# Kernel optimization log

Measured on AMD Instinct MI355X. Metric: run time of the kernel, lower is better.

Reference implementation:

```python
import jax, jax.numpy as jnp
import numpy as np
from jax import lax

DIM = 2048
N_HEADS = 16
N_KV = 4
HEAD_DIM = DIM // N_HEADS  # 128
ROPE_BASE = 10000.0
SEQ = 4096
BSZ = 1


def bitlinear(x, W):
    # per-row abs-mean scale (detached), ternary round/clamp, straight-through blend
    s = lax.stop_gradient(jnp.clip(jnp.mean(jnp.abs(W), axis=1, keepdims=True), 1e-5, None))
    wt = jnp.clip(jnp.round(W / s), -1.0, 1.0)
    w = lax.stop_gradient(wt - W) + W  # straight-through
    return x @ (w * s).T


def rms_norm(x):
    eps = jnp.finfo(x.dtype).eps
    return x * lax.rsqrt(jnp.mean(x * x, axis=-1, keepdims=True) + eps)


def rope(x, cos, sin):
    half = x.shape[-1] // 2
    x1, x2 = x[..., :half], x[..., half:]
    return jnp.concatenate((x1 * cos + x2 * sin, -x1 * sin + x2 * cos), axis=-1)


def setup_inputs() -> dict:
    key = jax.random.key(0)
    ks = jax.random.split(key, 6)
    kv_dim = N_KV * HEAD_DIM
    return {
        "x": jax.random.normal(ks[0], (BSZ, SEQ, DIM), dtype=jnp.float32),
        "wq": jax.random.normal(ks[1], (DIM, DIM), dtype=jnp.float32) * 0.02,
        "wk": jax.random.normal(ks[2], (kv_dim, DIM), dtype=jnp.float32) * 0.02,
        "wv": jax.random.normal(ks[3], (kv_dim, DIM), dtype=jnp.float32) * 0.02,
        "wp": jax.random.normal(ks[4], (DIM, DIM), dtype=jnp.float32) * 0.02,
        "q_gain": jnp.ones((N_HEADS,), dtype=jnp.float32),
    }


def reference(x, wq, wk, wv, wp, q_gain):
    b, s, d = x.shape
    q = bitlinear(x, wq).reshape(b, s, N_HEADS, HEAD_DIM).transpose(0, 2, 1, 3)  # bhsd
    k = bitlinear(x, wk).reshape(b, s, N_KV, HEAD_DIM).transpose(0, 2, 1, 3)
    v = bitlinear(x, wv).reshape(b, s, N_KV, HEAD_DIM).transpose(0, 2, 1, 3)

    q = rms_norm(q)
    k = rms_norm(k)

    inv_freq = 1.0 / ROPE_BASE ** (jnp.arange(0, HEAD_DIM, 2, dtype=jnp.float32) / HEAD_DIM)
    t = jnp.arange(s, dtype=jnp.float32)
    freqs = jnp.outer(t, inv_freq)  # [s, hd/2]
    cos = jnp.cos(freqs)[None, None].astype(q.dtype)
    sin = jnp.sin(freqs)[None, None].astype(q.dtype)
    q = rope(q, cos, sin)
    k = rope(k, cos, sin)

    q = q * q_gain.astype(q.dtype)[None, :, None, None]

    groups = N_HEADS // N_KV
    k = jnp.repeat(k, groups, axis=1)  # GQA expand to [b, H, s, hd]
    v = jnp.repeat(v, groups, axis=1)

    scale = 1.0 / np.sqrt(HEAD_DIM)
    scores = jnp.einsum("bhqd,bhkd->bhqk", q, k) * scale
    causal = jnp.tril(jnp.ones((s, s), dtype=bool))
    scores = jnp.where(causal[None, None], scores, jnp.finfo(scores.dtype).min)
    attn = jax.nn.softmax(scores, axis=-1)
    y = jnp.einsum("bhqk,bhkd->bhqd", attn, v)

    y = y.transpose(0, 2, 1, 3).reshape(b, s, d)
    return bitlinear(y, wp)
```

## Files before the change

### kernel.cpp

```cpp
#include <hip/hip_runtime.h>
#include <math.h>

typedef unsigned short u16;
typedef short s16x8 __attribute__((ext_vector_type(8)));
typedef short s16x4 __attribute__((ext_vector_type(4)));
typedef float f32x4 __attribute__((ext_vector_type(4)));
typedef u16 u16x4 __attribute__((ext_vector_type(4)));

static constexpr size_t OFF_XB   = 0;
static constexpr size_t OFF_WQKV = 16777216;
static constexpr size_t OFF_KH   = 16777216;
static constexpr size_t OFF_VT   = 20971520;
static constexpr size_t OFF_ML   = 25165824;
static constexpr size_t OFF_WP   = 29360128;
static constexpr size_t OFF_QKV  = 37748736;
static constexpr size_t OFF_Y    = 79691776;

__device__ __forceinline__ u16 f2bf(float f) {
  union { float f; unsigned u; } v; v.f = f;
  unsigned r = v.u + 0x7fffu + ((v.u >> 16) & 1u);
  return (u16)(r >> 16);
}

__device__ __forceinline__ float bf2f(u16 b) {
  union { unsigned u; float f; } v; v.u = ((unsigned)b) << 16;
  return v.f;
}

__device__ __forceinline__ void async16(const u16* g, u16* lds) {
  __builtin_amdgcn_global_load_lds(
      (const __attribute__((address_space(1))) void*)g,
      (__attribute__((address_space(3))) void*)lds, 16, 0, 0);
}

__global__ __launch_bounds__(256) void quant_all(const float* __restrict__ wq,
                                                 const float* __restrict__ wk,
                                                 const float* __restrict__ wv,
                                                 const float* __restrict__ wp,
                                                 u16* __restrict__ outqkv,
                                                 u16* __restrict__ outp) {
  const int row = blockIdx.x, tid = threadIdx.x;
  const float* src;
  u16* dst;
  if (row < 2048)      { src = wq + (size_t)row * 2048;          dst = outqkv + (size_t)row * 2048; }
  else if (row < 2560) { src = wk + (size_t)(row - 2048) * 2048; dst = outqkv + (size_t)row * 2048; }
  else if (row < 3072) { src = wv + (size_t)(row - 2560) * 2048; dst = outqkv + (size_t)row * 2048; }
  else                 { src = wp + (size_t)(row - 3072) * 2048; dst = outp + (size_t)(row - 3072) * 2048; }
  src += tid * 8;
  float4 a = *(const float4*)(src);
  float4 b = *(const float4*)(src + 4);
  float asum = fabsf(a.x)+fabsf(a.y)+fabsf(a.z)+fabsf(a.w)
             + fabsf(b.x)+fabsf(b.y)+fabsf(b.z)+fabsf(b.w);
  #pragma unroll
  for (int off = 1; off < 64; off <<= 1) asum += __shfl_xor(asum, off, 64);
  __shared__ float red[4];
  if ((tid & 63) == 0) red[tid >> 6] = asum;
  __syncthreads();
  float s = fmaxf((red[0]+red[1]+red[2]+red[3]) * (1.0f/2048.0f), 1e-5f);
  float v[8] = {a.x,a.y,a.z,a.w,b.x,b.y,b.z,b.w};
  u16* d = dst + tid * 8;
  #pragma unroll
  for (int i = 0; i < 8; i++) {
    float q = rintf(v[i] / s);
    q = fminf(fmaxf(q, -1.f), 1.f);
    d[i] = f2bf(q * s);
  }
}

__global__ __launch_bounds__(256) void cvt_bf16(const float* __restrict__ in,
                                                u16* __restrict__ out) {
  size_t i = ((size_t)blockIdx.x * 256 + threadIdx.x) * 4;
  float4 v = *(const float4*)(in + i);
  u16x4 o;
  o.x = f2bf(v.x); o.y = f2bf(v.y); o.z = f2bf(v.z); o.w = f2bf(v.w);
  *(u16x4*)(out + i) = o;
}

__global__ __launch_bounds__(256) void gemm_bt(const u16* __restrict__ A,
                                               const u16* __restrict__ B,
                                               float* __restrict__ C,
                                               int M, int N, int K) {
  __shared__ u16 sA[128 * 32];
  __shared__ u16 sB[128 * 32];
  const int tid = threadIdx.x;
  const int lane = tid & 63;
  const int wid = tid >> 6;
  const int lr = lane & 15, lq = lane >> 4;
  const int wm = (wid >> 1) * 64, wn = (wid & 1) * 64;
  const size_t m0 = (size_t)blockIdx.y * 128, n0 = (size_t)blockIdx.x * 128;

  const int r0 = tid >> 2, c0 = (tid & 3) * 8;
  const u16* Ab0 = A + (m0 + r0) * (size_t)K + c0;
  const u16* Ab1 = A + (m0 + 64 + r0) * (size_t)K + c0;
  const u16* Bb0 = B + (n0 + r0) * (size_t)K + c0;
  const u16* Bb1 = B + (n0 + 64 + r0) * (size_t)K + c0;
  u16* sA0 = &sA[tid * 8];
  u16* sA1 = &sA[(256 + tid) * 8];
  u16* sB0 = &sB[tid * 8];
  u16* sB1 = &sB[(256 + tid) * 8];

  f32x4 acc[4][4] = {};

  for (int kt = 0; kt < K; kt += 32) {
    async16(Ab0 + kt, sA0);
    async16(Ab1 + kt, sA1);
    async16(Bb0 + kt, sB0);
    async16(Bb1 + kt, sB1);
    __syncthreads();
    s16x8 af[4], bf[4];
    #pragma unroll
    for (int mt = 0; mt < 4; mt++)
      af[mt] = *(const s16x8*)&sA[(wm + mt * 16 + lr) * 32 + lq * 8];
    #pragma unroll
    for (int nt = 0; nt < 4; nt++)
      bf[nt] = *(const s16x8*)&sB[(wn + nt * 16 + lr) * 32 + lq * 8];
    #pragma unroll
    for (int mt = 0; mt < 4; mt++)
      #pragma unroll
      for (int nt = 0; nt < 4; nt++)
        acc[mt][nt] = __builtin_amdgcn_mfma_f32_16x16x32_bf16(af[mt], bf[nt], acc[mt][nt], 0, 0, 0);
    __syncthreads();
  }
  #pragma unroll
  for (int mt = 0; mt < 4; mt++)
    #pragma unroll
    for (int nt = 0; nt < 4; nt++)
      #pragma unroll
      for (int r = 0; r < 4; r++) {
        size_t m = m0 + wm + mt * 16 + lq * 4 + r;
        size_t n = n0 + wn + nt * 16 + lr;
        C[m * (size_t)N + n] = acc[mt][nt][r];
      }
}

__global__ __launch_bounds__(256) void prep_qk(const float* __restrict__ qkv,
                                               const float* __restrict__ qgain,
                                               u16* __restrict__ Qh,
                                               u16* __restrict__ Kh) {
  const int s = blockIdx.y;
  const int j = blockIdx.x * 4 + (threadIdx.x >> 6);
  const int t = threadIdx.x & 63;
  const float* row = qkv + (size_t)s * 3072 + (size_t)j * 128;
  float x1 = row[t], x2 = row[t + 64];
  float ss = x1 * x1 + x2 * x2;
  #pragma unroll
  for (int off = 1; off < 64; off <<= 1) ss += __shfl_xor(ss, off, 64);
  float rn = rsqrtf(ss * (1.0f / 128.0f) + 1.1920929e-07f);
  float invf = exp2f(-(float)t * 0.20762050593048096f);
  float ang = (float)s * invf;
  float sn, c;
  sincosf(ang, &sn, &c);
  if (j < 16) {
    float g = qgain[j] * 0.12751738f;
    float q1 = x1 * rn, q2 = x2 * rn;
    float o1 = (q1 * c + q2 * sn) * g;
    float o2 = (-q1 * sn + q2 * c) * g;
    u16* dst = Qh + ((size_t)j * 4096 + s) * 128;
    dst[t] = f2bf(o1); dst[t + 64] = f2bf(o2);
  } else {
    const int kvh = j - 16;
    float k1 = x1 * rn, k2 = x2 * rn;
    float o1 = k1 * c + k2 * sn;
    float o2 = -k1 * sn + k2 * c;
    const int tt = s >> 6, kr = s & 63;
    u16* base = Kh + (((size_t)kvh * 64 + tt) * 4) * 2048 + kr * 32 + (t & 31);
    base[(size_t)(t >> 5) * 2048]       = f2bf(o1);
    base[(size_t)(2 + (t >> 5)) * 2048] = f2bf(o2);
  }
}

__global__ __launch_bounds__(256) void vtrans(const float* __restrict__ qkv,
                                              u16* __restrict__ Vtg) {
  __shared__ float tile[64][67];
  const int tid = threadIdx.x;
  const int s0 = blockIdx.y * 64;
  const int c0 = blockIdx.x * 64;
  #pragma unroll
  for (int it = 0; it < 4; it++) {
    int i = it * 256 + tid;
    int r = i >> 4, c = (i & 15) * 4;
    float4 v = *(const float4*)(qkv + (size_t)(s0 + r) * 3072 + 2560 + c0 + c);
    tile[r][c] = v.x; tile[r][c + 1] = v.y; tile[r][c + 2] = v.z; tile[r][c + 3] = v.w;
  }
  __syncthreads();
  #pragma unroll
  for (int it = 0; it < 2; it++) {
    int i = it * 256 + tid;
    int dl = i >> 3, sc = (i & 7) * 8;
    int cglob = c0 + dl;
    int kvh = cglob >> 7, d = cglob & 127;
    int tt = s0 >> 6;
    int a0 = 16 * ((sc >> 2) & 3) + 4 * (sc >> 4);
    int a1 = 16 * (((sc >> 2) + 1) & 3) + 4 * (sc >> 4);
    int x = d & 7;
    int p0 = ((((a0 >> 3) ^ x) << 3) | (a0 & 7));
    int p1 = ((((a1 >> 3) ^ x) << 3) | (a1 & 7));
    size_t rowbase = (((size_t)kvh * 64 + tt) * 128 + d) * 64;
    u16 lo[4], hi[4];
    #pragma unroll
    for (int jj = 0; jj < 4; jj++) lo[jj] = f2bf(tile[sc + jj][dl]);
    #pragma unroll
    for (int jj = 0; jj < 4; jj++) hi[jj] = f2bf(tile[sc + 4 + jj][dl]);
    *(s16x4*)&Vtg[rowbase + p0] = *(s16x4*)lo;
    *(s16x4*)&Vtg[rowbase + p1] = *(s16x4*)hi;
  }
}

#define SEG(qt,a,b,s) ((unsigned)((qt)|((a)<<5)|((b)<<11)|((s)<<18)))
__constant__ unsigned SEGTAB[128] = {
  SEG(0,0,2,127),   SEG(15,0,15,14),
  SEG(15,15,32,15), 0,
  SEG(1,0,4,127),   SEG(14,0,13,12),
  SEG(14,13,30,13), 0,
  SEG(2,0,6,127),   SEG(13,0,11,10),
  SEG(13,11,28,11), 0,
  SEG(3,0,8,127),   SEG(12,0,9,8),
  SEG(12,9,26,9),   0,
  SEG(4,0,10,127),  SEG(11,0,7,6),
  SEG(11,7,24,7),   0,
  SEG(5,0,12,127),  SEG(10,0,5,4),
  SEG(10,5,22,5),   0,
  SEG(6,0,14,127),  SEG(9,0,3,2),
  SEG(9,3,20,3),    0,
  SEG(7,0,16,127),  SEG(8,0,1,0),
  SEG(8,1,18,1),    0,
  SEG(16,0,16,16),  0,
  SEG(16,16,33,17), 0,
  SEG(16,33,34,18), SEG(17,0,15,19),
  SEG(17,15,31,20), 0,
  SEG(17,31,36,21), SEG(18,0,12,22),
  SEG(18,12,28,23), 0,
  SEG(18,28,38,24), SEG(19,0,6,25),
  SEG(19,6,23,26),  0,
  SEG(19,23,39,27), 0,
  SEG(19,39,40,28), SEG(20,0,15,29),
  SEG(20,15,32,30), 0,
  SEG(20,32,42,31), SEG(21,0,6,32),
  SEG(21,6,22,33),  0,
  SEG(21,22,39,34), 0,
  SEG(21,39,44,35), SEG(22,0,11,36),
  SEG(22,11,27,37), 0,
  SEG(22,27,44,38), 0,
  SEG(22,44,46,39), SEG(23,0,14,40),
  SEG(23,14,30,41), 0,
  SEG(23,30,47,42), 0,
  SEG(23,47,48,43), SEG(24,0,15,44),
  SEG(24,15,31,45), 0,
  SEG(24,31,48,46), 0,
  SEG(24,48,50,47), SEG(25,0,14,48),
  SEG(25,14,30,49), 0,
  SEG(25,30,47,50), 0,
  SEG(25,47,52,51), SEG(26,0,11,52),
  SEG(26,11,27,53), 0,
  SEG(26,27,44,54), 0,
  SEG(26,44,54,55), SEG(27,0,6,56),
  SEG(27,6,22,57),  0,
  SEG(27,22,39,58), 0,
  SEG(27,39,55,59), 0,
  SEG(27,55,56,60), SEG(28,0,15,61),
  SEG(28,15,32,62), 0,
  SEG(28,32,48,63), 0,
  SEG(28,48,58,64), SEG(29,0,6,65),
  SEG(29,6,23,66),  0,
  SEG(29,23,39,67), 0,
  SEG(29,39,55,68), 0,
  SEG(29,55,60,69), SEG(30,0,12,70),
  SEG(30,12,28,71), 0,
  SEG(30,28,44,72), 0,
  SEG(30,44,61,73), 0,
  SEG(30,61,62,74), SEG(31,0,15,75),
  SEG(31,15,31,76), 0,
  SEG(31,31,48,77), 0,
  SEG(31,48,64,78), 0,
};
__constant__ unsigned char CBASE[24] = {0,2,4,6,8,10,12,14, 16,19,22,25,29,32,36,40, 44,48,52,56,61,65,70,75};
__constant__ unsigned char CCNT[24]  = {2,2,2,2,2,2,2,2, 3,3,3,4,3,4,4,4, 4,4,4,5,4,5,5,4};

__global__ __launch_bounds__(256, 2) void attn(const u16* __restrict__ Q,
                                               const u16* __restrict__ Kh,
                                               const u16* __restrict__ Vt,
                                               u16* __restrict__ Y,
                                               u16* __restrict__ Opart,
                                               float* __restrict__ MLpart) {
  const int tid = threadIdx.x, lane = tid & 63, wid = tid >> 6;
  const int lr = lane & 15, lq = lane >> 4;
  const int b = blockIdx.x;
  const int h = b & 15, unit = b >> 4;
  const int kvh = h >> 2;

  __shared__ u16 sK[4 * 64 * 32];
  __shared__ u16 sVt[128 * 64];

  const u16* Kbase = Kh + (size_t)kvh * 64 * 8192;
  const u16* Vbase = Vt + (size_t)kvh * 64 * 8192;

  const int o01 = (((2 * lq) ^ (lr & 7)) << 3);
  const int o23 = (((2 * lq + 1) ^ (lr & 7)) << 3);

  #pragma unroll 1
  for (int si = 0; si < 2; ++si) {
    const unsigned sd = SEGTAB[unit * 2 + si];
    const int qt = sd & 31;
    const int t0 = (sd >> 5) & 63;
    const int t1 = (sd >> 11) & 127;
    const int slot = (sd >> 18) & 127;
    if (t1 <= t0) continue;
    const int qbase = qt * 128;

    s16x8 qf[2][4];
    #pragma unroll
    for (int f = 0; f < 2; f++) {
      const u16* qp = Q + ((size_t)h * 4096 + qbase + wid * 32 + f * 16 + lr) * 128 + lq * 8;
      #pragma unroll
      for (int kc = 0; kc < 4; kc++) qf[f][kc] = *(const s16x8*)(qp + kc * 32);
    }

    f32x4 oacc[2][8] = {};
    f32x4 lacc[2] = {};
    float mrow[2] = {-1e30f, -1e30f};

    for (int t = t0; t < t1; ++t) {
      const u16* Kt = Kbase + (size_t)t * 8192;
      const u16* Vtt = Vbase + (size_t)t * 8192;
      #pragma unroll
      for (int it = 0; it < 4; it++) {
        int off = it * 2048 + tid * 8;
        async16(Kt + off, &sK[off]);
        async16(Vtt + off, &sVt[off]);
      }
      __syncthreads();

      f32x4 sacc[2][4] = {};
      #pragma unroll
      for (int nt = 0; nt < 4; nt++)
        #pragma unroll
        for (int kc = 0; kc < 4; kc++) {
          s16x8 kf = *(const s16x8*)&sK[kc * 2048 + (nt * 16 + lr) * 32 + lq * 8];
          sacc[0][nt] = __builtin_amdgcn_mfma_f32_16x16x32_bf16(kf, qf[0][kc], sacc[0][nt], 0, 0, 0);
          sacc[1][nt] = __builtin_amdgcn_mfma_f32_16x16x32_bf16(kf, qf[1][kc], sacc[1][nt], 0, 0, 0);
        }

      if (t >= 2 * qt) {
        #pragma unroll
        for (int f = 0; f < 2; f++) {
          int qg = qbase + wid * 32 + f * 16 + lr;
          #pragma unroll
          for (int nt = 0; nt < 4; nt++) {
            int kv0 = t * 64 + nt * 16 + lq * 4;
            #pragma unroll
            for (int r = 0; r < 4; r++)
              if (kv0 + r > qg) sacc[f][nt][r] = -1e30f;
          }
        }
      }

      float pm[2];
      #pragma unroll
      for (int f = 0; f < 2; f++) {
        float a = fmaxf(fmaxf(sacc[f][0][0], sacc[f][0][1]), fmaxf(sacc[f][0][2], sacc[f][0][3]));
        float bb = fmaxf(fmaxf(sacc[f][1][0], sacc[f][1][1]), fmaxf(sacc[f][1][2], sacc[f][1][3]));
        float cc = fmaxf(fmaxf(sacc[f][2][0], sacc[f][2][1]), fmaxf(sacc[f][2][2], sacc[f][2][3]));
        float dd = fmaxf(fmaxf(sacc[f][3][0], sacc[f][3][1]), fmaxf(sacc[f][3][2], sacc[f][3][3]));
        pm[f] = fmaxf(fmaxf(a, bb), fmaxf(cc, dd));
      }
      if (__any((pm[0] > mrow[0] + 3.0f) || (pm[1] > mrow[1] + 3.0f))) {
        #pragma unroll
        for (int f = 0; f < 2; f++) {
          float mn = pm[f];
          mn = fmaxf(mn, __shfl_xor(mn, 16, 64));
          mn = fmaxf(mn, __shfl_xor(mn, 32, 64));
          mn = fmaxf(mn, mrow[f]);
          float al = exp2f(mrow[f] - mn);
          mrow[f] = mn;
          lacc[f] *= al;
          #pragma unroll
          for (int dt = 0; dt < 8; dt++)
            #pragma unroll
            for (int r = 0; r < 4; r++) oacc[f][dt][r] *= al;
        }
      }

      s16x4 pf[2][4];
      #pragma unroll
      for (int f = 0; f < 2; f++)
        #pragma unroll
        for (int nt = 0; nt < 4; nt++)
          #pragma unroll
          for (int r = 0; r < 4; r++) {
            union { float fv; unsigned u; } pu;
            pu.fv = exp2f(sacc[f][nt][r] - mrow[f]);
            lacc[f][r] += pu.fv;
            pf[f][nt][r] = (short)(pu.u >> 16);
          }

      #pragma unroll
      for (int dt = 0; dt < 8; dt++) {
        const u16* vrow = &sVt[(dt * 16 + lr) * 64];
        s16x8 v01 = *(const s16x8*)(vrow + o01);
        s16x8 v23 = *(const s16x8*)(vrow + o23);
        s16x4 vf0 = {v01[0], v01[1], v01[2], v01[3]};
        s16x4 vf1 = {v01[4], v01[5], v01[6], v01[7]};
        s16x4 vf2 = {v23[0], v23[1], v23[2], v23[3]};
        s16x4 vf3 = {v23[4], v23[5], v23[6], v23[7]};
        #pragma unroll
        for (int f = 0; f < 2; f++) {
          oacc[f][dt] = __builtin_amdgcn_mfma_f32_16x16x16bf16_1k(vf0, pf[f][0], oacc[f][dt], 0, 0, 0);
          oacc[f][dt] = __builtin_amdgcn_mfma_f32_16x16x16bf16_1k(vf1, pf[f][1], oacc[f][dt], 0, 0, 0);
          oacc[f][dt] = __builtin_amdgcn_mfma_f32_16x16x16bf16_1k(vf2, pf[f][2], oacc[f][dt], 0, 0, 0);
          oacc[f][dt] = __builtin_amdgcn_mfma_f32_16x16x16bf16_1k(vf3, pf[f][3], oacc[f][dt], 0, 0, 0);
        }
      }
      __syncthreads();
    }

    float lrow[2];
    #pragma unroll
    for (int f = 0; f < 2; f++) {
      float s4 = (lacc[f][0] + lacc[f][1]) + (lacc[f][2] + lacc[f][3]);
      s4 += __shfl_xor(s4, 16, 64);
      s4 += __shfl_xor(s4, 32, 64);
      lrow[f] = s4;
    }

    if (slot == 127) {
      #pragma unroll
      for (int f = 0; f < 2; f++) {
        float linv = 1.0f / lrow[f];
        int qg = qbase + wid * 32 + f * 16 + lr;
        #pragma unroll
        for (int dt = 0; dt < 8; dt++) {
          u16 tmp[4];
          #pragma unroll
          for (int r = 0; r < 4; r++) tmp[r] = f2bf(oacc[f][dt][r] * linv);
          *(s16x4*)&Y[(size_t)qg * 2048 + h * 128 + dt * 16 + lq * 4] = *(s16x4*)tmp;
        }
      }
    } else {
      const int gslot = h * 79 + slot;
      u16* Op = Opart + (size_t)gslot * 16384;
      #pragma unroll
      for (int f = 0; f < 2; f++) {
        int row = wid * 32 + f * 16 + lr;
        #pragma unroll
        for (int dt = 0; dt < 8; dt++) {
          u16 tmp[4];
          #pragma unroll
          for (int r = 0; r < 4; r++) tmp[r] = f2bf(oacc[f][dt][r]);
          *(s16x4*)&Op[row * 128 + dt * 16 + lq * 4] = *(s16x4*)tmp;
        }
        if (lq == 0) {
          MLpart[(size_t)gslot * 256 + row * 2]     = mrow[f];
          MLpart[(size_t)gslot * 256 + row * 2 + 1] = lrow[f];
        }
      }
    }
  }
}

__global__ __launch_bounds__(256) void combine(const u16* __restrict__ Op,
                                               const float* __restrict__ ML,
                                               u16* __restrict__ Y) {
  const int b = blockIdx.x;
  const int qt = 8 + (b >> 4), h = b & 15;
  const int base = CBASE[qt - 8], n = CCNT[qt - 8];
  const int gbase = h * 79 + base;
  const int tid = threadIdx.x;
  const int row = tid >> 1, half = (tid & 1) * 64;

  float m[5], l[5];
  float mstar = -3e38f;
  for (int i = 0; i < n; i++) {
    m[i] = ML[(size_t)(gbase + i) * 256 + row * 2];
    l[i] = ML[(size_t)(gbase + i) * 256 + row * 2 + 1];
    mstar = fmaxf(mstar, m[i]);
  }
  float w[5], wsum = 0.f;
  for (int i = 0; i < n; i++) { w[i] = exp2f(m[i] - mstar); wsum += l[i] * w[i]; }
  float inv = 1.0f / wsum;

  float acc[64] = {};
  for (int i = 0; i < n; i++) {
    const u16* o = Op + (size_t)(gbase + i) * 16384 + row * 128 + half;
    float wi = w[i];
    #pragma unroll
    for (int c = 0; c < 64; c += 8) {
      s16x8 a = *(const s16x8*)(o + c);
      #pragma unroll
      for (int jj = 0; jj < 8; jj++) acc[c + jj] += wi * bf2f((u16)a[jj]);
    }
  }
  u16* dst = Y + ((size_t)qt * 128 + row) * 2048 + h * 128 + half;
  #pragma unroll
  for (int c = 0; c < 64; c += 8) {
    u16 tmp[8];
    #pragma unroll
    for (int jj = 0; jj < 8; jj++) tmp[jj] = f2bf(acc[c + jj] * inv);
    *(s16x8*)(dst + c) = *(s16x8*)tmp;
  }
}

extern "C" void kernel_launch(void* const* d_in, const int* in_sizes, int n_in,
                              void* d_out, int out_size, void* d_ws, size_t ws_size,
                              hipStream_t stream) {
  const float* x  = (const float*)d_in[0];
  const float* wq = (const float*)d_in[1];
  const float* wk = (const float*)d_in[2];
  const float* wv = (const float*)d_in[3];
  const float* wp = (const float*)d_in[4];
  const float* qg = (const float*)d_in[5];
  float* out = (float*)d_out;
  char* ws = (char*)d_ws;

  u16*   XB    = (u16*)(ws + OFF_XB);
  u16*   WQKV  = (u16*)(ws + OFF_WQKV);
  u16*   WP    = (u16*)(ws + OFF_WP);
  float* QKV   = (float*)(ws + OFF_QKV);
  u16*   QH    = XB;
  u16*   KH    = (u16*)(ws + OFF_KH);
  u16*   VT    = (u16*)(ws + OFF_VT);
  float* MLP   = (float*)(ws + OFF_ML);
  u16*   OPART = (u16*)(ws + OFF_QKV);
  u16*   Yb    = (u16*)(ws + OFF_Y);

  quant_all<<<5120, 256, 0, stream>>>(wq, wk, wv, wp, WQKV, WP);
  cvt_bf16<<<8192, 256, 0, stream>>>(x, XB);
  gemm_bt<<<dim3(24, 32), 256, 0, stream>>>(XB, WQKV, QKV, 4096, 3072, 2048);
  prep_qk<<<dim3(5, 4096), 256, 0, stream>>>(QKV, qg, QH, KH);
  vtrans<<<dim3(8, 64), 256, 0, stream>>>(QKV, VT);
  attn<<<1024, 256, 0, stream>>>(QH, KH, VT, Yb, OPART, MLP);
  combine<<<384, 256, 0, stream>>>(OPART, MLP, Yb);
  gemm_bt<<<dim3(16, 32), 256, 0, stream>>>(Yb, WP, out, 4096, 2048, 2048);
}
```

Baseline: 391.2 us.

## Double-buffer K/V tiles, swizzle K layout, use 16x16x32 MFMA for PV

```diff
diff --git a/kernel.cpp b/kernel.cpp
--- a/kernel.cpp
+++ b/kernel.cpp
@@ -149,7 +149,7 @@
   float invf = exp2f(-(float)t * 0.20762050593048096f);
   float ang = (float)s * invf;
   float sn, c;
-  sincosf(ang, &sn, &c);
+  __sincosf(ang, &sn, &c);
   if (j < 16) {
     float g = qgain[j] * 0.12751738f;
     float q1 = x1 * rn, q2 = x2 * rn;
@@ -163,9 +163,12 @@
     float o1 = k1 * c + k2 * sn;
     float o2 = -k1 * sn + k2 * c;
     const int tt = s >> 6, kr = s & 63;
-    u16* base = Kh + (((size_t)kvh * 64 + tt) * 4) * 2048 + kr * 32 + (t & 31);
-    base[(size_t)(t >> 5) * 2048]       = f2bf(o1);
-    base[(size_t)(2 + (t >> 5)) * 2048] = f2bf(o2);
+    const int sw = (kr >> 1) & 3;
+    u16* tile = Kh + ((size_t)kvh * 64 + tt) * 8192;
+    { int d = t;      int kc = d >> 5, gk = (d >> 3) & 3, e = d & 7;
+      tile[(kc * 256 + kr * 4 + (gk ^ sw)) * 8 + e] = f2bf(o1); }
+    { int d = t + 64; int kc = d >> 5, gk = (d >> 3) & 3, e = d & 7;
+      tile[(kc * 256 + kr * 4 + (gk ^ sw)) * 8 + e] = f2bf(o2); }
   }
 }
 
@@ -190,19 +193,19 @@
     int cglob = c0 + dl;
     int kvh = cglob >> 7, d = cglob & 127;
     int tt = s0 >> 6;
-    int a0 = 16 * ((sc >> 2) & 3) + 4 * (sc >> 4);
-    int a1 = 16 * (((sc >> 2) + 1) & 3) + 4 * (sc >> 4);
+    int qb = sc >> 3;
+    int glo = ((qb >> 1) & 1) * 4 + (qb & 1) * 2;
+    int ghi = glo + 1;
+    int ebase = ((qb >> 2) & 1) * 4;
     int x = d & 7;
-    int p0 = ((((a0 >> 3) ^ x) << 3) | (a0 & 7));
-    int p1 = ((((a1 >> 3) ^ x) << 3) | (a1 & 7));
     size_t rowbase = (((size_t)kvh * 64 + tt) * 128 + d) * 64;
     u16 lo[4], hi[4];
     #pragma unroll
     for (int jj = 0; jj < 4; jj++) lo[jj] = f2bf(tile[sc + jj][dl]);
     #pragma unroll
     for (int jj = 0; jj < 4; jj++) hi[jj] = f2bf(tile[sc + 4 + jj][dl]);
-    *(s16x4*)&Vtg[rowbase + p0] = *(s16x4*)lo;
-    *(s16x4*)&Vtg[rowbase + p1] = *(s16x4*)hi;
+    *(s16x4*)&Vtg[rowbase + (size_t)((glo ^ x) * 8 + ebase)] = *(s16x4*)lo;
+    *(s16x4*)&Vtg[rowbase + (size_t)((ghi ^ x) * 8 + ebase)] = *(s16x4*)hi;
   }
 }
 
@@ -288,14 +291,14 @@
   const int h = b & 15, unit = b >> 4;
   const int kvh = h >> 2;
 
-  __shared__ u16 sK[4 * 64 * 32];
-  __shared__ u16 sVt[128 * 64];
+  __shared__ u16 sKV[2][16384];
 
   const u16* Kbase = Kh + (size_t)kvh * 64 * 8192;
   const u16* Vbase = Vt + (size_t)kvh * 64 * 8192;
 
-  const int o01 = (((2 * lq) ^ (lr & 7)) << 3);
-  const int o23 = (((2 * lq + 1) ^ (lr & 7)) << 3);
+  const int kx8 = (lq ^ ((lr >> 1) & 3)) * 8;
+  const int vo0 = ((lq ^ (lr & 7)) << 3);
+  const int vo1 = (((4 + lq) ^ (lr & 7)) << 3);
 
   #pragma unroll 1
   for (int si = 0; si < 2; ++si) {
@@ -306,6 +309,18 @@
     const int slot = (sd >> 18) & 127;
     if (t1 <= t0) continue;
     const int qbase = qt * 128;
+    const int nst = t1 - t0;
+
+    {
+      const u16* Kt = Kbase + (size_t)t0 * 8192;
+      const u16* Vtt = Vbase + (size_t)t0 * 8192;
+      #pragma unroll
+      for (int it = 0; it < 4; it++) {
+        int off = it * 2048 + tid * 8;
+        async16(Kt + off, &sKV[0][off]);
+        async16(Vtt + off, &sKV[0][8192 + off]);
+      }
+    }
 
     s16x8 qf[2][4];
     #pragma unroll
@@ -319,26 +334,39 @@
     f32x4 lacc[2] = {};
     float mrow[2] = {-1e30f, -1e30f};
 
-    for (int t = t0; t < t1; ++t) {
-      const u16* Kt = Kbase + (size_t)t * 8192;
-      const u16* Vtt = Vbase + (size_t)t * 8192;
-      #pragma unroll
-      for (int it = 0; it < 4; it++) {
-        int off = it * 2048 + tid * 8;
-        async16(Kt + off, &sK[off]);
-        async16(Vtt + off, &sVt[off]);
-      }
-      __syncthreads();
+    for (int t2 = 0; t2 < nst; ++t2) {
+      const int t = t0 + t2;
+      const int cur = t2 & 1;
+      if (t2 + 1 < nst) {
+        const u16* Kt = Kbase + (size_t)(t + 1) * 8192;
+        const u16* Vtt = Vbase + (size_t)(t + 1) * 8192;
+        u16* dstb = &sKV[cur ^ 1][0];
+        #pragma unroll
+        for (int it = 0; it < 4; it++) {
+          int off = it * 2048 + tid * 8;
+          async16(Kt + off, dstb + off);
+          async16(Vtt + off, dstb + 8192 + off);
+        }
+        asm volatile("s_waitcnt vmcnt(8)" ::: "memory");
+      } else {
+        asm volatile("s_waitcnt vmcnt(0)" ::: "memory");
+      }
+      asm volatile("s_barrier" ::: "memory");
+
+      const u16* bufK = &sKV[cur][0];
+      const u16* bufV = &sKV[cur][8192];
 
       f32x4 sacc[2][4] = {};
       #pragma unroll
-      for (int nt = 0; nt < 4; nt++)
+      for (int nt = 0; nt < 4; nt++) {
+        const int rowoff = (nt * 16 + lr) * 32 + kx8;
         #pragma unroll
         for (int kc = 0; kc < 4; kc++) {
-          s16x8 kf = *(const s16x8*)&sK[kc * 2048 + (nt * 16 + lr) * 32 + lq * 8];
+          s16x8 kf = *(const s16x8*)&bufK[kc * 2048 + rowoff];
           sacc[0][nt] = __builtin_amdgcn_mfma_f32_16x16x32_bf16(kf, qf[0][kc], sacc[0][nt], 0, 0, 0);
           sacc[1][nt] = __builtin_amdgcn_mfma_f32_16x16x32_bf16(kf, qf[1][kc], sacc[1][nt], 0, 0, 0);
         }
+      }
 
       if (t >= 2 * qt) {
         #pragma unroll
@@ -380,37 +408,32 @@
         }
       }
 
-      s16x4 pf[2][4];
+      s16x8 pf[2][2];
       #pragma unroll
       for (int f = 0; f < 2; f++)
         #pragma unroll
-        for (int nt = 0; nt < 4; nt++)
+        for (int c = 0; c < 2; c++)
           #pragma unroll
-          for (int r = 0; r < 4; r++) {
+          for (int j = 0; j < 8; j++) {
+            int nt = 2 * (j >> 2) + c;
+            int r = j & 3;
             union { float fv; unsigned u; } pu;
             pu.fv = exp2f(sacc[f][nt][r] - mrow[f]);
             lacc[f][r] += pu.fv;
-            pf[f][nt][r] = (short)(pu.u >> 16);
+            pf[f][c][j] = (short)(pu.u >> 16);
           }
 
       #pragma unroll
       for (int dt = 0; dt < 8; dt++) {
-        const u16* vrow = &sVt[(dt * 16 + lr) * 64];
-        s16x8 v01 = *(const s16x8*)(vrow + o01);
-        s16x8 v23 = *(const s16x8*)(vrow + o23);
-        s16x4 vf0 = {v01[0], v01[1], v01[2], v01[3]};
-        s16x4 vf1 = {v01[4], v01[5], v01[6], v01[7]};
-        s16x4 vf2 = {v23[0], v23[1], v23[2], v23[3]};
-        s16x4 vf3 = {v23[4], v23[5], v23[6], v23[7]};
-        #pragma unroll
-        for (int f = 0; f < 2; f++) {
-          oacc[f][dt] = __builtin_amdgcn_mfma_f32_16x16x16bf16_1k(vf0, pf[f][0], oacc[f][dt], 0, 0, 0);
-          oacc[f][dt] = __builtin_amdgcn_mfma_f32_16x16x16bf16_1k(vf1, pf[f][1], oacc[f][dt], 0, 0, 0);
-          oacc[f][dt] = __builtin_amdgcn_mfma_f32_16x16x16bf16_1k(vf2, pf[f][2], oacc[f][dt], 0, 0, 0);
-          oacc[f][dt] = __builtin_amdgcn_mfma_f32_16x16x16bf16_1k(vf3, pf[f][3], oacc[f][dt], 0, 0, 0);
-        }
-      }
-      __syncthreads();
+        const u16* vrow = bufV + (dt * 16 + lr) * 64;
+        s16x8 va0 = *(const s16x8*)(vrow + vo0);
+        s16x8 va1 = *(const s16x8*)(vrow + vo1);
+        oacc[0][dt] = __builtin_amdgcn_mfma_f32_16x16x32_bf16(va0, pf[0][0], oacc[0][dt], 0, 0, 0);
+        oacc[1][dt] = __builtin_amdgcn_mfma_f32_16x16x32_bf16(va0, pf[1][0], oacc[1][dt], 0, 0, 0);
+        oacc[0][dt] = __builtin_amdgcn_mfma_f32_16x16x32_bf16(va1, pf[0][1], oacc[0][dt], 0, 0, 0);
+        oacc[1][dt] = __builtin_amdgcn_mfma_f32_16x16x32_bf16(va1, pf[1][1], oacc[1][dt], 0, 0, 0);
+      }
+      asm volatile("s_waitcnt lgkmcnt(0)\n\ts_barrier" ::: "memory");
     }
 
     float lrow[2];
```

Result: faster. 378.0 us (-3.4%).
